# Kernel optimization log

Measured on AMD Instinct MI355X. Metric: run time of the kernel, lower is better.

The kernel has to match this reference:

```python
import jax, jax.numpy as jnp
import numpy as np

WORD_DIM = 300
HIDDEN = 768
B, S = 128, 256
H_DIR = HIDDEN // 2          # 384 per-direction LSTM hidden
SEMA = HIDDEN // 3 * 2       # 512
STRU = HIDDEN // 3           # 256
EPS_MT = 1.0                 # MatrixTree eps


def setup_inputs() -> dict:
    key = jax.random.key(0)
    ks = jax.random.split(key, 18)
    rn = lambda k, shp, s=1.0: jax.random.normal(k, shp, dtype=jnp.float32) * s
    s_l = 1.0 / np.sqrt(H_DIR)
    s_d = 1.0 / np.sqrt(STRU)
    return {
        'input': rn(ks[0], (B, S, WORD_DIM)),
        'mask': jnp.ones((B, S, 1), jnp.float32),
        # forward-direction LSTM (PyTorch gate order i,f,g,o)
        'w_ih_f': rn(ks[1], (4 * H_DIR, WORD_DIM), s_l),
        'w_hh_f': rn(ks[2], (4 * H_DIR, H_DIR), s_l),
        'b_f': rn(ks[3], (4 * H_DIR,), s_l),
        # backward-direction LSTM
        'w_ih_b': rn(ks[4], (4 * H_DIR, WORD_DIM), s_l),
        'w_hh_b': rn(ks[5], (4 * H_DIR, H_DIR), s_l),
        'b_b': rn(ks[6], (4 * H_DIR,), s_l),
        # structured attention params
        'w_tp': rn(ks[7], (STRU, STRU), s_d),
        'b_tp': rn(ks[8], (STRU,), s_d),
        'w_tc': rn(ks[9], (STRU, STRU), s_d),
        'b_tc': rn(ks[10], (STRU,), s_d),
        'w_a': rn(ks[11], (STRU, STRU), 0.02),  # scaled so exp(scores) stays finite
        'w_root': rn(ks[12], (1, STRU), s_d),
        'root_emb': rn(ks[13], (SEMA,)),
        'w_r': rn(ks[14], (SEMA, SEMA * 3), 1.0 / np.sqrt(3 * SEMA)),
        'b_r': rn(ks[15], (SEMA,), 1.0 / np.sqrt(3 * SEMA)),
    }


def _lstm_dir(x, w_ih, w_hh, b):
    # x: [S, B, E] -> hs: [S, B, H]
    h0 = jnp.zeros((x.shape[1], w_hh.shape[1]), x.dtype)
    def step(carry, xt):
        h, c = carry
        g = xt @ w_ih.T + h @ w_hh.T + b
        i, f, gg, o = jnp.split(g, 4, axis=-1)
        c = jax.nn.sigmoid(f) * c + jax.nn.sigmoid(i) * jnp.tanh(gg)
        h = jax.nn.sigmoid(o) * jnp.tanh(c)
        return (h, c), h
    _, hs = jax.lax.scan(step, (h0, h0), x)
    return hs


def _matrix_tree(A, r):
    # A: [B,S,S] (zero diagonal), r: [B,S,1]
    bsz, seq_len = A.shape[0], A.shape[1]
    idx = jnp.arange(seq_len)
    L = -A
    L = L.at[:, idx, idx].set(A.sum(axis=1))          # column sums on diagonal
    LL = jnp.concatenate([r[..., 0][:, None, :], L[:, 1:, :]], axis=1)
    dg = LL[:, idx, idx]
    LL = LL.at[:, idx, idx].set(jnp.where(dg == 0, EPS_MT, dg))
    LL_inv = jnp.linalg.inv(LL)
    d0 = (r[..., 0] * LL_inv[:, :, 0])[:, None, :]     # [B,1,S]
    diag_inv = LL_inv[:, idx, idx]                     # [B,S]
    term1 = A * diag_inv[:, None, :]                   # A[i,j] * inv_diag[j]
    term2 = A * jnp.swapaxes(LL_inv, 1, 2)             # A[i,j] * inv[j,i]
    term1 = term1.at[:, :, 0].set(0.0)
    term2 = term2.at[:, 0, :].set(0.0)
    return d0, term1 - term2


def reference(input, mask, w_ih_f, w_hh_f, b_f, w_ih_b, w_hh_b, b_b,
              w_tp, b_tp, w_tc, b_tc, w_a, w_root, root_emb, w_r, b_r):
    bsz, seq_len = input.shape[0], input.shape[1]
    xs = jnp.swapaxes(input, 0, 1)                     # [S,B,E]
    hf = _lstm_dir(xs, w_ih_f, w_hh_f, b_f)            # [S,B,H_DIR]
    hb = _lstm_dir(xs[::-1], w_ih_b, w_hh_b, b_b)[::-1]
    out = jnp.swapaxes(jnp.concatenate([hf, hb], axis=-1), 0, 1)  # [B,S,2H]
    of_, ob = out[..., :H_DIR], out[..., H_DIR:]
    half = SEMA // 2
    vec_sema = jnp.concatenate([of_[..., :half], ob[..., :half]], axis=-1)  # [B,S,SEMA]
    vec_stru = jnp.concatenate([of_[..., half:], ob[..., half:]], axis=-1)  # [B,S,STRU]

    tp = jnp.tanh(vec_stru @ w_tp.T + b_tp)
    tc = jnp.tanh(vec_stru @ w_tc.T + b_tc)
    mask_sq = jnp.einsum('bsi,bti->bst', mask, mask)
    f = jnp.einsum('bsd,de,bte->bst', tp, w_a, tc)
    f = jnp.exp(f) * mask_sq
    f_r = jnp.exp(vec_stru @ w_root.T) * mask          # [B,S,1]
    idx = jnp.arange(seq_len)
    f = f.at[:, idx, idx].set(0.0)

    a0, a = _matrix_tree(f, f_r)                       # [B,1,S], [B,S,S]
    a_c = a
    a_p = jnp.swapaxes(jnp.concatenate([a0, a], axis=1), 1, 2)  # [B,S,S+1]

    root_embs = jnp.broadcast_to(root_emb, (bsz, 1, SEMA))
    vec_sem_root = jnp.concatenate([root_embs, vec_sema], axis=1)  # [B,S+1,SEMA]
    c = a_c @ vec_sema                                  # [B,S,SEMA]
    p = a_p @ vec_sem_root                              # [B,S,SEMA]
    output = jnp.tanh(jnp.concatenate([vec_sema, p, c], axis=-1) @ w_r.T + b_r)
    output = output * mask
    emb = output.max(axis=1)                            # [B,SEMA]
    return emb, output
```

## Files before the change

kernel.cpp:

```cpp
#include <hip/hip_runtime.h>
#include <hip/hip_fp16.h>
#include <math.h>

#define B_    128
#define S_    256
#define WORD_ 300
#define HD_   384
#define M_    32768
#define STRU_ 256
#define SEMA_ 512
#define SEG   16777216L

typedef __half half_t;
typedef _Float16 f16x8 __attribute__((ext_vector_type(8)));
typedef float    f32x4 __attribute__((ext_vector_type(4)));

template<bool BNN>
__global__ __launch_bounds__(256)
void mgemm(const half_t* __restrict__ Ag, const half_t* __restrict__ Bg,
           half_t* __restrict__ Cg,
           int M, int N, int K, int lda, int ldb, int ldc,
           long sA, long sB, long sC,
           const float* __restrict__ bias, int act,
           const float* __restrict__ d0v, const float* __restrict__ rootv)
{
    __shared__ __half As[128][40];
    __shared__ __half Bs[64][40];
    const int bz = blockIdx.z;
    const half_t* A  = Ag + (long)bz * sA;
    const half_t* Bp = Bg + (long)bz * sB;
    const int m0 = blockIdx.y * 128, n0 = blockIdx.x * 64;
    const int tid = threadIdx.x;
    const int l = tid & 63, w = tid >> 6;
    const int wm = w & 1, wn = w >> 1;
    const int lr = l & 15, lq = l >> 4;

    f32x4 acc[4][2] = {};

    for (int k0 = 0; k0 < K; k0 += 32) {
        #pragma unroll
        for (int i = 0; i < 2; i++) {
            int ch = tid + i * 256;
            int r = ch >> 2, j = ch & 3;
            *(float4*)&As[r][j * 8] = *(const float4*)(A + (long)(m0 + r) * lda + k0 + j * 8);
        }
        if (!BNN) {
            int r = tid >> 2, j = tid & 3;
            *(float4*)&Bs[r][j * 8] = *(const float4*)(Bp + (long)(n0 + r) * ldb + k0 + j * 8);
        } else {
            int k = tid & 31, nc = tid >> 5;
            float4 v = *(const float4*)(Bp + (long)(k0 + k) * ldb + n0 + nc * 8);
            const __half* hv = (const __half*)&v;
            #pragma unroll
            for (int jj = 0; jj < 8; jj++) Bs[nc * 8 + jj][k] = hv[jj];
        }
        __syncthreads();

        f16x8 af[4], bf[2];
        #pragma unroll
        for (int mf = 0; mf < 4; mf++)
            af[mf] = *(const f16x8*)&As[wm * 64 + mf * 16 + lr][lq * 8];
        #pragma unroll
        for (int nf = 0; nf < 2; nf++)
            bf[nf] = *(const f16x8*)&Bs[wn * 32 + nf * 16 + lr][lq * 8];
        #pragma unroll
        for (int mf = 0; mf < 4; mf++)
            #pragma unroll
            for (int nf = 0; nf < 2; nf++)
                acc[mf][nf] = __builtin_amdgcn_mfma_f32_16x16x32_f16(af[mf], bf[nf], acc[mf][nf], 0, 0, 0);
        __syncthreads();
    }

    #pragma unroll
    for (int mf = 0; mf < 4; mf++) {
        #pragma unroll
        for (int nf = 0; nf < 2; nf++) {
            #pragma unroll
            for (int j = 0; j < 4; j++) {
                int m = m0 + wm * 64 + mf * 16 + lq * 4 + j;
                int n = n0 + wn * 32 + nf * 16 + lr;
                float v = acc[mf][nf][j];
                if (bias) v += bias[n];
                if (d0v)  v += d0v[(long)bz * M + m] * rootv[n];
                if (act == 1)      v = tanhf(v);
                else if (act == 2) v = (m == n) ? 0.f : expf(v);
                Cg[(long)bz * sC + (long)m * ldc + n] = __float2half(v);
            }
        }
    }
}

__global__ __launch_bounds__(256)
void mgemm_final(const half_t* __restrict__ A0, const half_t* __restrict__ A1,
                 const half_t* __restrict__ A2, const half_t* __restrict__ Bw,
                 float* __restrict__ Cout, const float* __restrict__ bias,
                 const float* __restrict__ maskp)
{
    __shared__ __half As[128][40];
    __shared__ __half Bs[64][40];
    const int m0 = blockIdx.y * 128, n0 = blockIdx.x * 64;
    const int tid = threadIdx.x;
    const int l = tid & 63, w = tid >> 6;
    const int wm = w & 1, wn = w >> 1;
    const int lr = l & 15, lq = l >> 4;

    f32x4 acc[4][2] = {};

    for (int k0 = 0; k0 < 1536; k0 += 32) {
        const half_t* A = (k0 < 512) ? A0 : (k0 < 1024) ? A1 : A2;
        const int kk = k0 & 511;
        #pragma unroll
        for (int i = 0; i < 2; i++) {
            int ch = tid + i * 256;
            int r = ch >> 2, j = ch & 3;
            *(float4*)&As[r][j * 8] = *(const float4*)(A + (long)(m0 + r) * 512 + kk + j * 8);
        }
        {
            int r = tid >> 2, j = tid & 3;
            *(float4*)&Bs[r][j * 8] = *(const float4*)(Bw + (long)(n0 + r) * 1536 + k0 + j * 8);
        }
        __syncthreads();
        f16x8 af[4], bf[2];
        #pragma unroll
        for (int mf = 0; mf < 4; mf++)
            af[mf] = *(const f16x8*)&As[wm * 64 + mf * 16 + lr][lq * 8];
        #pragma unroll
        for (int nf = 0; nf < 2; nf++)
            bf[nf] = *(const f16x8*)&Bs[wn * 32 + nf * 16 + lr][lq * 8];
        #pragma unroll
        for (int mf = 0; mf < 4; mf++)
            #pragma unroll
            for (int nf = 0; nf < 2; nf++)
                acc[mf][nf] = __builtin_amdgcn_mfma_f32_16x16x32_f16(af[mf], bf[nf], acc[mf][nf], 0, 0, 0);
        __syncthreads();
    }

    #pragma unroll
    for (int mf = 0; mf < 4; mf++) {
        #pragma unroll
        for (int nf = 0; nf < 2; nf++) {
            #pragma unroll
            for (int j = 0; j < 4; j++) {
                int m = m0 + wm * 64 + mf * 16 + lq * 4 + j;
                int n = n0 + wn * 32 + nf * 16 + lr;
                float v = tanhf(acc[mf][nf][j] + bias[n]) * maskp[m];
                Cout[(long)m * 512 + n] = v;
            }
        }
    }
}

__global__ __launch_bounds__(256)
void ggemm(const float* __restrict__ x, const half_t* __restrict__ Wp,
           const float* __restrict__ bp, half_t* __restrict__ G, int chunk)
{
    __shared__ __half As[128][40];
    __shared__ __half Bs[128][40];
    const int d = blockIdx.z;
    const int ts = blockIdx.y;
    const int m0 = blockIdx.x * 128;
    const int t_orig = d ? (255 - (chunk * 128 + ts)) : (chunk * 128 + ts);
    const int tid = threadIdx.x;
    const int l = tid & 63, w = tid >> 6;
    const int wm = w & 1, wn = w >> 1;
    const int lr = l & 15, lq = l >> 4;

    f32x4 acc[4][4] = {};

    for (int k0 = 0; k0 < 320; k0 += 32) {
        #pragma unroll
        for (int i = 0; i < 2; i++) {
            int e = tid + i * 256;
            int r = e >> 2, j = (e & 3) * 8;
            *(float4*)&As[r][j] = *(const float4*)(Wp + ((long)d * 1536 + m0 + r) * 320 + k0 + j);
        }
        #pragma unroll
        for (int i = 0; i < 2; i++) {
            int e = tid + i * 256;
            int r = e >> 2, j = (e & 3) * 8;
            int k = k0 + j;
            int ka = (k + 4 <= 300) ? k : 0;
            int kb = (k + 8 <= 300) ? k + 4 : 0;
            const float* xp = x + ((long)r * 256 + t_orig) * 300;
            float4 va = *(const float4*)(xp + ka);
            float4 vb = *(const float4*)(xp + kb);
            __half* q = &Bs[r][j];
            q[0] = __float2half(va.x); q[1] = __float2half(va.y);
            q[2] = __float2half(va.z); q[3] = __float2half(va.w);
            q[4] = __float2half(vb.x); q[5] = __float2half(vb.y);
            q[6] = __float2half(vb.z); q[7] = __float2half(vb.w);
        }
        __syncthreads();
        f16x8 af[4], bf[4];
        #pragma unroll
        for (int gf = 0; gf < 4; gf++)
            af[gf] = *(const f16x8*)&As[wm * 64 + gf * 16 + lr][lq * 8];
        #pragma unroll
        for (int bi = 0; bi < 4; bi++)
            bf[bi] = *(const f16x8*)&Bs[wn * 64 + bi * 16 + lr][lq * 8];
        #pragma unroll
        for (int gf = 0; gf < 4; gf++)
            #pragma unroll
            for (int bi = 0; bi < 4; bi++)
                acc[gf][bi] = __builtin_amdgcn_mfma_f32_16x16x32_f16(af[gf], bf[bi], acc[gf][bi], 0, 0, 0);
        __syncthreads();
    }

    half_t* Gt = G + (long)(ts * 2 + d) * 196608;
    #pragma unroll
    for (int gf = 0; gf < 4; gf++) {
        #pragma unroll
        for (int bi = 0; bi < 4; bi++) {
            int g = m0 + wm * 64 + gf * 16 + lq * 4;
            int b = wn * 64 + bi * 16 + lr;
            union { __half h[4]; float2 f; } u;
            #pragma unroll
            for (int j = 0; j < 4; j++)
                u.h[j] = __float2half(acc[gf][bi][j] + bp[d * 1536 + g + j]);
            *(float2*)(Gt + ((long)(g >> 2) * 128 + b) * 4) = u.f;
        }
    }
}

__global__ __launch_bounds__(256)
void lstm_scan(const half_t* __restrict__ G, const half_t* __restrict__ Whh,
               half_t* __restrict__ Hbuf, float* __restrict__ Cst,
               half_t* __restrict__ vs, half_t* __restrict__ vst,
               unsigned* __restrict__ flags, int chunk)
{
    __shared__ __half Wl[64 * 392];
    __shared__ __half hlo[16][68];

    const int bid = blockIdx.x;
    const int d = bid / 48, rem = bid % 48;
    const int ntile = rem >> 1, btile = rem & 1;
    const int grp = d * 2 + btile;
    const int tid = threadIdx.x;
    const int l = tid & 63, w = tid >> 6;
    const int wm = w & 1, wn = w >> 1;
    const int lr = l & 15, lq = l >> 4;

    {
        const half_t* src = Whh + ((long)d * 1536 + ntile * 64) * 384;
        for (int e = tid; e < 3072; e += 256) {
            int r = e / 48, c = (e % 48) * 8;
            *(float4*)&Wl[r * 392 + c] = *(const float4*)(src + (long)r * 384 + c);
        }
    }
    float creg[4];
    if (chunk == 0) {
        creg[0] = creg[1] = creg[2] = creg[3] = 0.f;
    } else {
        #pragma unroll
        for (int i = 0; i < 4; i++) creg[i] = Cst[((long)bid * 256 + tid) * 4 + i];
    }

    const int bg0 = btile * 64 + wn * 32 + lr;
    long goff[4];
    #pragma unroll
    for (int gf = 0; gf < 2; gf++)
        #pragma unroll
        for (int bf2 = 0; bf2 < 2; bf2++) {
            const int hdg = ntile * 16 + wm * 8 + gf * 4 + lq;
            const int bg  = bg0 + bf2 * 16;
            goff[gf * 2 + bf2] = ((long)hdg * 128 + bg) * 4;
        }
    float2 gc0, gc1, gc2, gc3;
    {
        const half_t* gp0 = G + (long)(0 * 2 + d) * 196608;
        gc0 = *(const float2*)(gp0 + goff[0]);
        gc1 = *(const float2*)(gp0 + goff[1]);
        gc2 = *(const float2*)(gp0 + goff[2]);
        gc3 = *(const float2*)(gp0 + goff[3]);
    }
    __syncthreads();

    union U16 { unsigned long long u[2]; f16x8 v; };

    for (int s = 0; s < 128; ++s) {
        const int gstep = chunk * 128 + s;
        const int p = gstep & 1;
        const half_t* hin = Hbuf + (long)(p * 2 + d) * 128 * 384;

        float2 gn0, gn1, gn2, gn3;
        {
            const int sn = (s < 127) ? s + 1 : 127;
            const half_t* gpn = G + (long)(sn * 2 + d) * 196608;
            gn0 = *(const float2*)(gpn + goff[0]);
            gn1 = *(const float2*)(gpn + goff[1]);
            gn2 = *(const float2*)(gpn + goff[2]);
            gn3 = *(const float2*)(gpn + goff[3]);
        }

        f16x8 hb[12][2];
        #pragma unroll
        for (int it = 0; it < 12; ++it)
            #pragma unroll
            for (int bf2 = 0; bf2 < 2; bf2++) {
                const unsigned long long* hp = (const unsigned long long*)
                    (hin + (long)(bg0 + bf2 * 16) * 384 + it * 32 + lq * 8);
                U16 t;
                t.u[0] = __hip_atomic_load(hp,     __ATOMIC_RELAXED, __HIP_MEMORY_SCOPE_AGENT);
                t.u[1] = __hip_atomic_load(hp + 1, __ATOMIC_RELAXED, __HIP_MEMORY_SCOPE_AGENT);
                hb[it][bf2] = t.v;
            }

        f32x4 acc[2][2] = {};
        #pragma unroll
        for (int it = 0; it < 12; ++it) {
            f16x8 af[2];
            #pragma unroll
            for (int gf = 0; gf < 2; gf++)
                af[gf] = *(const f16x8*)&Wl[(wm * 32 + gf * 16 + lr) * 392 + it * 32 + lq * 8];
            #pragma unroll
            for (int gf = 0; gf < 2; gf++)
                #pragma unroll
                for (int bf2 = 0; bf2 < 2; bf2++)
                    acc[gf][bf2] = __builtin_amdgcn_mfma_f32_16x16x32_f16(af[gf], hb[it][bf2], acc[gf][bf2], 0, 0, 0);
        }

        #pragma unroll
        for (int gf = 0; gf < 2; gf++) {
            #pragma unroll
            for (int bf2 = 0; bf2 < 2; bf2++) {
                const int hd_l = wm * 8 + gf * 4 + lq;
                const int bl_  = wn * 32 + bf2 * 16 + lr;
                union { float2 f; __half h[4]; } gu;
                const int ci = gf * 2 + bf2;
                gu.f = (ci == 0) ? gc0 : (ci == 1) ? gc1 : (ci == 2) ? gc2 : gc3;
                float gi  = acc[gf][bf2][0] + __half2float(gu.h[0]);
                float gfo = acc[gf][bf2][1] + __half2float(gu.h[1]);
                float gg  = acc[gf][bf2][2] + __half2float(gu.h[2]);
                float go  = acc[gf][bf2][3] + __half2float(gu.h[3]);
                float c = creg[ci];
                float si = 1.f / (1.f + expf(-gi));
                float sf = 1.f / (1.f + expf(-gfo));
                float so = 1.f / (1.f + expf(-go));
                c = sf * c + si * tanhf(gg);
                creg[ci] = c;
                hlo[hd_l][bl_] = __float2half(so * tanhf(c));
            }
        }
        __syncthreads();

        if (tid < 128) {
            const int b_l = tid & 63, h8 = tid >> 6;
            f16x8 v;
            #pragma unroll
            for (int j = 0; j < 8; j++) v[j] = (_Float16)hlo[h8 * 8 + j][b_l];
            const int bg_w  = btile * 64 + b_l;
            const int hd0_w = ntile * 16 + h8 * 8;
            U16 sv; sv.v = v;
            unsigned long long* hp = (unsigned long long*)
                (Hbuf + ((long)((p ^ 1) * 2 + d) * 128 + bg_w) * 384 + hd0_w);
            __hip_atomic_store(hp,     sv.u[0], __ATOMIC_RELAXED, __HIP_MEMORY_SCOPE_AGENT);
            __hip_atomic_store(hp + 1, sv.u[1], __ATOMIC_RELAXED, __HIP_MEMORY_SCOPE_AGENT);
            const int t_orig = d ? 255 - gstep : gstep;
            const long m = (long)bg_w * 256 + t_orig;
            if (hd0_w < 256)
                __builtin_nontemporal_store(v, (f16x8*)(vs + m * 512 + d * 256 + hd0_w));
            else
                __builtin_nontemporal_store(v, (f16x8*)(vst + m * 256 + d * 128 + (hd0_w - 256)));
        }

        if (s < 127) {
            __syncthreads();
            if (tid == 0)
                __hip_atomic_store(&flags[(grp * 24 + ntile) * 16], (unsigned)(gstep + 1),
                                   __ATOMIC_RELAXED, __HIP_MEMORY_SCOPE_AGENT);
            const unsigned tgt = (unsigned)(gstep + 1);
            const unsigned fidx = (grp * 24 + (l % 24)) * 16;
            while (true) {
                unsigned fv = __hip_atomic_load(&flags[fidx], __ATOMIC_RELAXED,
                                                __HIP_MEMORY_SCOPE_AGENT);
                if (__all(fv >= tgt)) break;
                __builtin_amdgcn_s_sleep(1);
            }
            asm volatile("" ::: "memory");
        }
        gc0 = gn0; gc1 = gn1; gc2 = gn2; gc3 = gn3;
    }

    #pragma unroll
    for (int i = 0; i < 4; i++) Cst[((long)bid * 256 + tid) * 4 + i] = creg[i];
}

__global__ void pack_wih(const float* __restrict__ wf, const float* __restrict__ wb,
                         const float* __restrict__ bfv, const float* __restrict__ bbv,
                         half_t* __restrict__ Wp, float* __restrict__ bp)
{
    int i = blockIdx.x * 256 + threadIdx.x;
    if (i < 983040) {
        int k = i % 320, pr = (i / 320) % 1536, d = i / 491520;
        int q = pr & 3, hd = pr >> 2;
        float v = (k < 300) ? (d ? wb : wf)[(q * 384 + hd) * 300 + k] : 0.f;
        Wp[i] = __float2half(v);
    }
    if (i < 3072) {
        int d = i / 1536, pr = i % 1536;
        int q = pr & 3, hd = pr >> 2;
        bp[i] = (d ? bbv : bfv)[q * 384 + hd];
    }
}
__global__ void pack_whh(const float* __restrict__ wf, const float* __restrict__ wb,
                         half_t* __restrict__ Wh)
{
    int i = blockIdx.x * 256 + threadIdx.x;
    if (i >= 1179648) return;
    int k = i % 384, pr = (i / 384) % 1536, d = i / 589824;
    int q = pr & 3, hd = pr >> 2;
    Wh[i] = __float2half((d ? wb : wf)[(q * 384 + hd) * 384 + k]);
}
__global__ void conv16(const float* __restrict__ s, half_t* __restrict__ d, long n)
{
    long i = (long)blockIdx.x * 256 + threadIdx.x;
    if (i < n) d[i] = __float2half(s[i]);
}
__global__ void convT16(const float* __restrict__ s, half_t* __restrict__ d, int R, int C)
{
    int i = blockIdx.x * 256 + threadIdx.x;
    if (i >= R * C) return;
    int r = i / C, c = i % C;
    d[(long)c * R + r] = __float2half(s[i]);
}

__global__ __launch_bounds__(256)
void frow_kernel(const half_t* __restrict__ vst, const float* __restrict__ wroot,
                 float* __restrict__ fr)
{
    int row  = blockIdx.x * 4 + (threadIdx.x >> 6);
    int lane = threadIdx.x & 63;
    const half_t* v = vst + (long)row * 256;
    float s = 0.f;
    for (int k = lane; k < 256; k += 64) s += __half2float(v[k]) * wroot[k];
    #pragma unroll
    for (int off = 32; off; off >>= 1) s += __shfl_down(s, off);
    if (lane == 0) fr[row] = expf(s);
}

__global__ __launch_bounds__(1024)
void invert_gj(const half_t* __restrict__ fA, const float* __restrict__ fr,
               half_t* __restrict__ LLinv)
{
    __shared__ float colbuf[2][256];
    __shared__ float rowbuf[2][256];
    __shared__ float csum[4][256];
    const int bz = blockIdx.x;
    const half_t* A = fA + (long)bz * 65536;
    const int tid = threadIdx.x;
    const int c = tid & 255, rh = tid >> 8;
    float m[64];

    float s = 0.f;
    #pragma unroll
    for (int i = 0; i < 64; i++) {
        float v = __half2float(A[(long)(rh * 64 + i) * 256 + c]);
        m[i] = v; s += v;
    }
    csum[rh][c] = s;
    __syncthreads();
    float diag = csum[0][c] + csum[1][c] + csum[2][c] + csum[3][c];
    const float frv = fr[bz * 256 + c];
    #pragma unroll
    for (int i = 0; i < 64; i++) {
        int r = rh * 64 + i;
        float v = (r == c) ? ((diag == 0.f) ? 1.f : diag) : -m[i];
        if (rh == 0 && i == 0) {
            v = frv;
            if (c == 0 && v == 0.f) v = 1.f;
        }
        m[i] = v;
    }
    __syncthreads();

    for (int k = 0; k < 256; k++) {
        const int p = k & 1;
        const int kh = k >> 6, kl = k & 63;
        if (c == k) {
            #pragma unroll
            for (int i = 0; i < 64; i++) colbuf[p][rh * 64 + i] = m[i];
        }
        if (rh == kh) {
            float pv = 0.f;
            #pragma unroll
            for (int i = 0; i < 64; i++) pv = (i == kl) ? m[i] : pv;
            rowbuf[p][c] = pv;
        }
        __syncthreads();
        const float piv  = colbuf[p][k];
        const float pinv = 1.f / piv;
        const float rv   = rowbuf[p][c] * pinv;
        if (c == k) {
            #pragma unroll
            for (int i = 0; i < 64; i++) m[i] = -colbuf[p][rh * 64 + i] * pinv;
        } else {
            #pragma unroll
            for (int i = 0; i < 64; i++) m[i] -= colbuf[p][rh * 64 + i] * rv;
        }
        if (rh == kh) {
            const float dv = (c == k) ? pinv : rv;
            #pragma unroll
            for (int i = 0; i < 64; i++) m[i] = (i == kl) ? dv : m[i];
        }
    }

    #pragma unroll
    for (int i = 0; i < 64; i++)
        LLinv[(long)bz * 65536 + (long)(rh * 64 + i) * 256 + c] = __float2half(m[i]);
}

__global__ void diag_d0_k(const half_t* __restrict__ LLinv, const float* __restrict__ fr,
                          float* __restrict__ diagv, float* __restrict__ d0)
{
    int i = blockIdx.x * 256 + threadIdx.x;
    if (i >= 32768) return;
    int b = i >> 8, s = i & 255;
    diagv[i] = __half2float(LLinv[(long)b * 65536 + s * 257]);
    d0[i]    = fr[i] * __half2float(LLinv[(long)b * 65536 + s * 256]);
}

__global__ __launch_bounds__(256)
void assemble_a(half_t* __restrict__ fA, const half_t* __restrict__ LLinv,
                const float* __restrict__ diagv)
{
    __shared__ float ll[32][33];
    const int bz = blockIdx.z;
    const int s0 = (blockIdx.x >> 3) * 32, t0 = (blockIdx.x & 7) * 32;
    const int tid = threadIdx.x;
    const long base = (long)bz * 65536;
    #pragma unroll
    for (int it = 0; it < 4; it++) {
        int i = (tid >> 5) + it * 8, j = tid & 31;
        ll[i][j] = __half2float(LLinv[base + (long)(t0 + i) * 256 + (s0 + j)]);
    }
    __syncthreads();
    #pragma unroll
    for (int it = 0; it < 4; it++) {
        int si = (tid >> 5) + it * 8, tj = tid & 31;
        int s = s0 + si, t = t0 + tj;
        long idx = base + (long)s * 256 + t;
        float Av = __half2float(fA[idx]);
        float t1 = (t > 0) ? diagv[(bz << 8) + t] : 0.f;
        float t2 = (s > 0) ? ll[tj][si] : 0.f;
        fA[idx] = __float2half(Av * (t1 - t2));
    }
}

__global__ __launch_bounds__(256)
void transpose256h(const half_t* __restrict__ in, half_t* __restrict__ out)
{
    __shared__ __half tb[32][33];
    const int bz = blockIdx.z;
    const half_t* ip = in  + (long)bz * 65536;
    half_t*       op = out + (long)bz * 65536;
    int x0 = blockIdx.x * 32, y0 = blockIdx.y * 32;
    int tx = threadIdx.x, ty = threadIdx.y;
    #pragma unroll
    for (int r = 0; r < 4; r++)
        tb[ty + 8 * r][tx] = ip[(long)(y0 + ty + 8 * r) * 256 + x0 + tx];
    __syncthreads();
    #pragma unroll
    for (int r = 0; r < 4; r++)
        op[(long)(x0 + ty + 8 * r) * 256 + y0 + tx] = tb[tx][ty + 8 * r];
}

__global__ __launch_bounds__(256)
void emb_max(const float* __restrict__ outp, float* __restrict__ emb)
{
    int b = blockIdx.x;
    for (int n = threadIdx.x; n < 512; n += 256) {
        const float* p = outp + (long)b * 131072 + n;
        float mx = -3.4e38f;
        for (int t = 0; t < 256; t++) mx = fmaxf(mx, p[(long)t * 512]);
        emb[b * 512 + n] = mx;
    }
}

__global__ void diag_ws(float* out, int n, float v)
{
    int i = blockIdx.x * 256 + threadIdx.x;
    if (i < n) out[i] = v;
}

extern "C" void kernel_launch(void* const* d_in, const int* in_sizes, int n_in,
                              void* d_out, int out_size, void* d_ws, size_t ws_size,
                              hipStream_t stream)
{
    const float* x     = (const float*)d_in[0];
    const float* mask  = (const float*)d_in[1];
    const float* wihf  = (const float*)d_in[2];
    const float* whhf  = (const float*)d_in[3];
    const float* bf    = (const float*)d_in[4];
    const float* wihb  = (const float*)d_in[5];
    const float* whhb  = (const float*)d_in[6];
    const float* bb    = (const float*)d_in[7];
    const float* wtp   = (const float*)d_in[8];
    const float* btp   = (const float*)d_in[9];
    const float* wtc   = (const float*)d_in[10];
    const float* btc   = (const float*)d_in[11];
    const float* wa    = (const float*)d_in[12];
    const float* wroot = (const float*)d_in[13];
    const float* remb  = (const float*)d_in[14];
    const float* wr    = (const float*)d_in[15];
    const float* br    = (const float*)d_in[16];

    if (ws_size < 134217728ULL) {
        float enc = 100.0f + (float)((double)ws_size * 1e-9);
        diag_ws<<<dim3((out_size + 255) / 256), 256, 0, stream>>>((float*)d_out, out_size, enc);
        return;
    }

    char* ws = (char*)d_ws;
    half_t* G     = (half_t*)(ws + 0);
    half_t* vs    = (half_t*)(ws + 100663296);
    half_t* tp    = (half_t*)(ws + 0 * SEG);
    half_t* tc    = (half_t*)(ws + 1 * SEG);
    half_t* tmp   = (half_t*)(ws + 2 * SEG);
    half_t* fA    = (half_t*)(ws + 3 * SEG);
    half_t* LL    = (half_t*)(ws + 4 * SEG);
    half_t* aT    = (half_t*)(ws + 5 * SEG);
    half_t* cbuf  = (half_t*)(ws + 0 * SEG);
    half_t* pbuf  = (half_t*)(ws + 2 * SEG);
    half_t* wr16  = (half_t*)(ws + 4 * SEG);

    float* ob = (float*)d_out;
    half_t*   Wp16  = (half_t*)(ob + 11000000);
    half_t*   Whh16 = (half_t*)(ob + 11491520);
    float*    bp    = ob + 12081344;
    half_t*   wtp16 = (half_t*)(ob + 12084416);
    half_t*   wtc16 = (half_t*)(ob + 12117184);
    half_t*   wa16T = (half_t*)(ob + 12149952);
    float*    fr    = ob + 12182720;
    float*    d0    = ob + 12215488;
    float*    diagv = ob + 12248256;
    float*    Cst   = ob + 12281024;
    half_t*   Hbuf  = (half_t*)(ob + 12379328);
    unsigned* flags = (unsigned*)(ob + 12500000);
    half_t*   vst   = (half_t*)(ob + 12648448);

    float* emb  = (float*)d_out;
    float* outp = (float*)d_out + 65536;

    hipMemsetAsync(Hbuf, 0, 393216, stream);
    hipMemsetAsync(flags, 0, 6144, stream);
    pack_wih<<<dim3(3840), 256, 0, stream>>>(wihf, wihb, bf, bb, Wp16, bp);
    pack_whh<<<dim3(4608), 256, 0, stream>>>(whhf, whhb, Whh16);
    conv16<<<dim3(256), 256, 0, stream>>>(wtp, wtp16, 65536);
    conv16<<<dim3(256), 256, 0, stream>>>(wtc, wtc16, 65536);
    convT16<<<dim3(256), 256, 0, stream>>>(wa, wa16T, 256, 256);

    for (int c = 0; c < 2; c++) {
        ggemm<<<dim3(12, 128, 2), 256, 0, stream>>>(x, Wp16, bp, G, c);
        lstm_scan<<<dim3(96), 256, 0, stream>>>(G, Whh16, Hbuf, Cst, vs, vst, flags, c);
    }

    frow_kernel<<<dim3(8192), 256, 0, stream>>>(vst, wroot, fr);

    mgemm<false><<<dim3(4, 256, 1), 256, 0, stream>>>(
        vst, wtp16, tp, M_, 256, 256, 256, 256, 256, 0, 0, 0, btp, 1, nullptr, nullptr);
    mgemm<false><<<dim3(4, 256, 1), 256, 0, stream>>>(
        vst, wtc16, tc, M_, 256, 256, 256, 256, 256, 0, 0, 0, btc, 1, nullptr, nullptr);

    mgemm<false><<<dim3(4, 256, 1), 256, 0, stream>>>(
        tp, wa16T, tmp, M_, 256, 256, 256, 256, 256, 0, 0, 0, nullptr, 0, nullptr, nullptr);

    mgemm<false><<<dim3(4, 2, 128), 256, 0, stream>>>(
        tmp, tc, fA, 256, 256, 256, 256, 256, 256, 65536, 65536, 65536,
        nullptr, 2, nullptr, nullptr);

    invert_gj<<<dim3(128), 1024, 0, stream>>>(fA, fr, LL);
    diag_d0_k<<<dim3(128), 256, 0, stream>>>(LL, fr, diagv, d0);
    assemble_a<<<dim3(64, 1, 128), 256, 0, stream>>>(fA, LL, diagv);

    conv16<<<dim3(3072), 256, 0, stream>>>(wr, wr16, 786432);

    transpose256h<<<dim3(8, 8, 128), dim3(32, 8), 0, stream>>>(fA, aT);

    mgemm<true><<<dim3(8, 2, 128), 256, 0, stream>>>(
        fA, vs, cbuf, 256, 512, 256, 256, 512, 512, 65536, 131072, 131072,
        nullptr, 0, nullptr, nullptr);

    mgemm<true><<<dim3(8, 2, 128), 256, 0, stream>>>(
        aT, vs, pbuf, 256, 512, 256, 256, 512, 512, 65536, 131072, 131072,
        nullptr, 0, d0, remb);

    mgemm_final<<<dim3(8, 256, 1), 256, 0, stream>>>(vs, pbuf, cbuf, wr16, outp, br, mask);

    emb_max<<<dim3(128), 256, 0, stream>>>(outp, emb);
}
```

Measured before the change: 3.380 ms.

## Keep LSTM recurrent weights in registers and halve persistent scan blocks

The persistent LSTM scan kernel now runs 48 blocks of 512 threads instead of 96 blocks of 256. Each block owns twice as many hidden units, and each wave keeps its W_hh fragments in VGPRs instead of reading them from LDS every step. The per-step h loads are interleaved with the MFMAs instead of being prefetched all at once. The progress flag is now published before the nontemporal output stores, and fewer blocks take part in each barrier. This is meant to cut LDS traffic and grid-barrier latency on the serial critical path, at the cost of heavy register pressure and half as many CUs doing work.

```diff
diff --git a/kernel.cpp b/kernel.cpp
--- a/kernel.cpp
+++ b/kernel.cpp
@@ -222,37 +222,37 @@
     }
 }
 
-__global__ __launch_bounds__(256)
+__global__ __launch_bounds__(512, 1)
 void lstm_scan(const half_t* __restrict__ G, const half_t* __restrict__ Whh,
                half_t* __restrict__ Hbuf, float* __restrict__ Cst,
                half_t* __restrict__ vs, half_t* __restrict__ vst,
                unsigned* __restrict__ flags, int chunk)
 {
-    __shared__ __half Wl[64 * 392];
-    __shared__ __half hlo[16][68];
+    __shared__ __half hlo[32][68];
 
     const int bid = blockIdx.x;
-    const int d = bid / 48, rem = bid % 48;
+    const int d = bid / 24, rem = bid % 24;
     const int ntile = rem >> 1, btile = rem & 1;
     const int grp = d * 2 + btile;
     const int tid = threadIdx.x;
     const int l = tid & 63, w = tid >> 6;
-    const int wm = w & 1, wn = w >> 1;
+    const int wm = w & 3, wn = w >> 2;
     const int lr = l & 15, lq = l >> 4;
 
-    {
-        const half_t* src = Whh + ((long)d * 1536 + ntile * 64) * 384;
-        for (int e = tid; e < 3072; e += 256) {
-            int r = e / 48, c = (e % 48) * 8;
-            *(float4*)&Wl[r * 392 + c] = *(const float4*)(src + (long)r * 384 + c);
-        }
-    }
+    f16x8 wf[12][2];
+    #pragma unroll
+    for (int it = 0; it < 12; it++)
+        #pragma unroll
+        for (int gf = 0; gf < 2; gf++)
+            wf[it][gf] = *(const f16x8*)(Whh +
+                ((long)d * 1536 + ntile * 128 + wm * 32 + gf * 16 + lr) * 384 + it * 32 + lq * 8);
+
     float creg[4];
     if (chunk == 0) {
         creg[0] = creg[1] = creg[2] = creg[3] = 0.f;
     } else {
         #pragma unroll
-        for (int i = 0; i < 4; i++) creg[i] = Cst[((long)bid * 256 + tid) * 4 + i];
+        for (int i = 0; i < 4; i++) creg[i] = Cst[((long)bid * 512 + tid) * 4 + i];
     }
 
     const int bg0 = btile * 64 + wn * 32 + lr;
@@ -261,7 +261,7 @@
     for (int gf = 0; gf < 2; gf++)
         #pragma unroll
         for (int bf2 = 0; bf2 < 2; bf2++) {
-            const int hdg = ntile * 16 + wm * 8 + gf * 4 + lq;
+            const int hdg = ntile * 32 + wm * 8 + gf * 4 + lq;
             const int bg  = bg0 + bf2 * 16;
             goff[gf * 2 + bf2] = ((long)hdg * 128 + bg) * 4;
         }
@@ -292,9 +292,10 @@
             gn3 = *(const float2*)(gpn + goff[3]);
         }
 
-        f16x8 hb[12][2];
-        #pragma unroll
-        for (int it = 0; it < 12; ++it)
+        f32x4 acc[2][2] = {};
+        #pragma unroll
+        for (int it = 0; it < 12; ++it) {
+            f16x8 hb[2];
             #pragma unroll
             for (int bf2 = 0; bf2 < 2; bf2++) {
                 const unsigned long long* hp = (const unsigned long long*)
@@ -302,21 +303,13 @@
                 U16 t;
                 t.u[0] = __hip_atomic_load(hp,     __ATOMIC_RELAXED, __HIP_MEMORY_SCOPE_AGENT);
                 t.u[1] = __hip_atomic_load(hp + 1, __ATOMIC_RELAXED, __HIP_MEMORY_SCOPE_AGENT);
-                hb[it][bf2] = t.v;
+                hb[bf2] = t.v;
             }
-
-        f32x4 acc[2][2] = {};
-        #pragma unroll
-        for (int it = 0; it < 12; ++it) {
-            f16x8 af[2];
-            #pragma unroll
-            for (int gf = 0; gf < 2; gf++)
-                af[gf] = *(const f16x8*)&Wl[(wm * 32 + gf * 16 + lr) * 392 + it * 32 + lq * 8];
             #pragma unroll
             for (int gf = 0; gf < 2; gf++)
                 #pragma unroll
                 for (int bf2 = 0; bf2 < 2; bf2++)
-                    acc[gf][bf2] = __builtin_amdgcn_mfma_f32_16x16x32_f16(af[gf], hb[it][bf2], acc[gf][bf2], 0, 0, 0);
+                    acc[gf][bf2] = __builtin_amdgcn_mfma_f32_16x16x32_f16(wf[it][gf], hb[bf2], acc[gf][bf2], 0, 0, 0);
         }
 
         #pragma unroll
@@ -343,18 +336,25 @@
         }
         __syncthreads();
 
-        if (tid < 128) {
+        f16x8 v;
+        int bg_w = 0, hd0_w = 0;
+        if (tid < 256) {
             const int b_l = tid & 63, h8 = tid >> 6;
-            f16x8 v;
             #pragma unroll
             for (int j = 0; j < 8; j++) v[j] = (_Float16)hlo[h8 * 8 + j][b_l];
-            const int bg_w  = btile * 64 + b_l;
-            const int hd0_w = ntile * 16 + h8 * 8;
+            bg_w  = btile * 64 + b_l;
+            hd0_w = ntile * 32 + h8 * 8;
             U16 sv; sv.v = v;
             unsigned long long* hp = (unsigned long long*)
                 (Hbuf + ((long)((p ^ 1) * 2 + d) * 128 + bg_w) * 384 + hd0_w);
             __hip_atomic_store(hp,     sv.u[0], __ATOMIC_RELAXED, __HIP_MEMORY_SCOPE_AGENT);
             __hip_atomic_store(hp + 1, sv.u[1], __ATOMIC_RELAXED, __HIP_MEMORY_SCOPE_AGENT);
+        }
+        __syncthreads();
+        if (s < 127 && tid == 0)
+            __hip_atomic_store(&flags[(grp * 12 + ntile) * 16], (unsigned)(gstep + 1),
+                               __ATOMIC_RELAXED, __HIP_MEMORY_SCOPE_AGENT);
+        if (tid < 256) {
             const int t_orig = d ? 255 - gstep : gstep;
             const long m = (long)bg_w * 256 + t_orig;
             if (hd0_w < 256)
@@ -364,12 +364,8 @@
         }
 
         if (s < 127) {
-            __syncthreads();
-            if (tid == 0)
-                __hip_atomic_store(&flags[(grp * 24 + ntile) * 16], (unsigned)(gstep + 1),
-                                   __ATOMIC_RELAXED, __HIP_MEMORY_SCOPE_AGENT);
             const unsigned tgt = (unsigned)(gstep + 1);
-            const unsigned fidx = (grp * 24 + (l % 24)) * 16;
+            const unsigned fidx = (grp * 12 + (l % 12)) * 16;
             while (true) {
                 unsigned fv = __hip_atomic_load(&flags[fidx], __ATOMIC_RELAXED,
                                                 __HIP_MEMORY_SCOPE_AGENT);
@@ -382,7 +378,7 @@
     }
 
     #pragma unroll
-    for (int i = 0; i < 4; i++) Cst[((long)bid * 256 + tid) * 4 + i] = creg[i];
+    for (int i = 0; i < 4; i++) Cst[((long)bid * 512 + tid) * 4 + i] = creg[i];
 }
 
 __global__ void pack_wih(const float* __restrict__ wf, const float* __restrict__ wb,
@@ -651,7 +647,7 @@
 
     for (int c = 0; c < 2; c++) {
         ggemm<<<dim3(12, 128, 2), 256, 0, stream>>>(x, Wp16, bp, G, c);
-        lstm_scan<<<dim3(96), 256, 0, stream>>>(G, Whh16, Hbuf, Cst, vs, vst, flags, c);
+        lstm_scan<<<dim3(48), 512, 0, stream>>>(G, Whh16, Hbuf, Cst, vs, vst, flags, c);
     }
 
     frow_kernel<<<dim3(8192), 256, 0, stream>>>(vst, wroot, fr);
```

Result: slower. 4.878 ms (+44.3%).

## Publish LSTM step flag before output stores; fuse transpose into assemble_a

Applied to the files above, without the earlier changes.

In the persistent LSTM recurrence, the per-step ready flag is now raised right after the hidden-state atomic stores and a barrier. The nontemporal stores of the sequence outputs happen after that, so the cross-block wait no longer includes them. Separately, assemble_a writes the transposed attention matrix from shared memory, which removes the standalone transpose kernel and one full read of fA. The cost is an extra barrier per step in the recurrence and slightly more shared memory in assemble_a.

```diff
diff --git a/kernel.cpp b/kernel.cpp
--- a/kernel.cpp
+++ b/kernel.cpp
@@ -343,18 +343,25 @@
         }
         __syncthreads();
 
+        f16x8 v;
+        int bg_w = 0, hd0_w = 0;
         if (tid < 128) {
             const int b_l = tid & 63, h8 = tid >> 6;
-            f16x8 v;
             #pragma unroll
             for (int j = 0; j < 8; j++) v[j] = (_Float16)hlo[h8 * 8 + j][b_l];
-            const int bg_w  = btile * 64 + b_l;
-            const int hd0_w = ntile * 16 + h8 * 8;
+            bg_w  = btile * 64 + b_l;
+            hd0_w = ntile * 16 + h8 * 8;
             U16 sv; sv.v = v;
             unsigned long long* hp = (unsigned long long*)
                 (Hbuf + ((long)((p ^ 1) * 2 + d) * 128 + bg_w) * 384 + hd0_w);
             __hip_atomic_store(hp,     sv.u[0], __ATOMIC_RELAXED, __HIP_MEMORY_SCOPE_AGENT);
             __hip_atomic_store(hp + 1, sv.u[1], __ATOMIC_RELAXED, __HIP_MEMORY_SCOPE_AGENT);
+        }
+        __syncthreads();
+        if (s < 127 && tid == 0)
+            __hip_atomic_store(&flags[(grp * 24 + ntile) * 16], (unsigned)(gstep + 1),
+                               __ATOMIC_RELAXED, __HIP_MEMORY_SCOPE_AGENT);
+        if (tid < 128) {
             const int t_orig = d ? 255 - gstep : gstep;
             const long m = (long)bg_w * 256 + t_orig;
             if (hd0_w < 256)
@@ -364,10 +371,6 @@
         }
 
         if (s < 127) {
-            __syncthreads();
-            if (tid == 0)
-                __hip_atomic_store(&flags[(grp * 24 + ntile) * 16], (unsigned)(gstep + 1),
-                                   __ATOMIC_RELAXED, __HIP_MEMORY_SCOPE_AGENT);
             const unsigned tgt = (unsigned)(gstep + 1);
             const unsigned fidx = (grp * 24 + (l % 24)) * 16;
             while (true) {
@@ -521,9 +524,10 @@
 
 __global__ __launch_bounds__(256)
 void assemble_a(half_t* __restrict__ fA, const half_t* __restrict__ LLinv,
-                const float* __restrict__ diagv)
-{
-    __shared__ float ll[32][33];
+                const float* __restrict__ diagv, half_t* __restrict__ aT)
+{
+    __shared__ float  ll[32][33];
+    __shared__ __half av[32][33];
     const int bz = blockIdx.z;
     const int s0 = (blockIdx.x >> 3) * 32, t0 = (blockIdx.x & 7) * 32;
     const int tid = threadIdx.x;
@@ -542,26 +546,16 @@
         float Av = __half2float(fA[idx]);
         float t1 = (t > 0) ? diagv[(bz << 8) + t] : 0.f;
         float t2 = (s > 0) ? ll[tj][si] : 0.f;
-        fA[idx] = __float2half(Av * (t1 - t2));
-    }
-}
-
-__global__ __launch_bounds__(256)
-void transpose256h(const half_t* __restrict__ in, half_t* __restrict__ out)
-{
-    __shared__ __half tb[32][33];
-    const int bz = blockIdx.z;
-    const half_t* ip = in  + (long)bz * 65536;
-    half_t*       op = out + (long)bz * 65536;
-    int x0 = blockIdx.x * 32, y0 = blockIdx.y * 32;
-    int tx = threadIdx.x, ty = threadIdx.y;
-    #pragma unroll
-    for (int r = 0; r < 4; r++)
-        tb[ty + 8 * r][tx] = ip[(long)(y0 + ty + 8 * r) * 256 + x0 + tx];
+        __half hv = __float2half(Av * (t1 - t2));
+        fA[idx] = hv;
+        av[si][tj] = hv;
+    }
     __syncthreads();
     #pragma unroll
-    for (int r = 0; r < 4; r++)
-        op[(long)(x0 + ty + 8 * r) * 256 + y0 + tx] = tb[tx][ty + 8 * r];
+    for (int it = 0; it < 4; it++) {
+        int ti = (tid >> 5) + it * 8, sj = tid & 31;
+        aT[base + (long)(t0 + ti) * 256 + (s0 + sj)] = av[sj][ti];
+    }
 }
 
 __global__ __launch_bounds__(256)
@@ -670,11 +664,9 @@
 
     invert_gj<<<dim3(128), 1024, 0, stream>>>(fA, fr, LL);
     diag_d0_k<<<dim3(128), 256, 0, stream>>>(LL, fr, diagv, d0);
-    assemble_a<<<dim3(64, 1, 128), 256, 0, stream>>>(fA, LL, diagv);
+    assemble_a<<<dim3(64, 1, 128), 256, 0, stream>>>(fA, LL, diagv, aT);
 
     conv16<<<dim3(3072), 256, 0, stream>>>(wr, wr16, 786432);
-
-    transpose256h<<<dim3(8, 8, 128), dim3(32, 8), 0, stream>>>(fA, aT);
 
     mgemm<true><<<dim3(8, 2, 128), 256, 0, stream>>>(
         fA, vs, cbuf, 256, 512, 256, 256, 512, 512, 65536, 131072, 131072,
```

Result: no change. 3.334 ms (-1.4%).
